# Kernel optimization log

Hardware: AMD Instinct MI355X
Metric: run time of the kernel (lower is better)

Reference implementation:

```python
import jax, jax.numpy as jnp
import numpy as np

FPS, MS = 7, 256
WIDTHS = [(FPS, 12), (12, 12), (12, 12), (12, 12), (12, 12), (12, 6), (6, 1)]


def setup_inputs() -> dict:
    key = jax.random.key(0)
    keys = jax.random.split(key, 1 + 2 * len(WIDTHS))
    B = 32768
    inp = {"inputs": jax.random.normal(keys[0], (B, MS, FPS), dtype=jnp.float32)}
    for li, (fan_in, fan_out) in enumerate(WIDTHS):
        scale = 1.0 / np.sqrt(fan_in)
        inp[f"W{li}"] = jax.random.uniform(keys[1 + 2 * li], (fan_in, fan_out), dtype=jnp.float32, minval=-scale, maxval=scale)
        inp[f"b{li}"] = jnp.zeros((fan_out,), dtype=jnp.float32)
    return inp


def _mlp(x, Ws, bs):
    # layer 0: linear activation
    h = x @ Ws[0] + bs[0]
    # layers 1-4: relu
    for li in range(1, 5):
        h = jax.nn.relu(h @ Ws[li] + bs[li])
    # layer 5: linear (6 units), layer 6: final linear (1 unit)
    h = h @ Ws[5] + bs[5]
    h = h @ Ws[6] + bs[6]
    return h


def reference(inputs, W0, b0, W1, b1, W2, b2, W3, b3, W4, b4, W5, b5, W6, b6):
    B = inputs.shape[0]
    Ws = [W0, W1, W2, W3, W4, W5, W6]
    bs = [b0, b1, b2, b3, b4, b5, b6]
    # Equivalent to looping over ms slices with the shared MLP then concatenating:
    # fold the ms dim into the batch, run once, reshape back to [B, ms].
    x = inputs.reshape(B * MS, FPS)
    out = _mlp(x, Ws, bs)  # [B*MS, 1]
    return out.reshape(B, MS)
```

## Files before the change

### kernel.cpp

```cpp
#include <hip/hip_runtime.h>

#define R 4
#define NTHREADS 256


__global__ __launch_bounds__(NTHREADS, 4) void mlp_kernel(
    const float* __restrict__ in,
    const float* __restrict__ W0, const float* __restrict__ b0,
    const float* __restrict__ W1, const float* __restrict__ b1,
    const float* __restrict__ W2, const float* __restrict__ b2,
    const float* __restrict__ W3, const float* __restrict__ b3,
    const float* __restrict__ W4, const float* __restrict__ b4,
    const float* __restrict__ W5, const float* __restrict__ b5,
    const float* __restrict__ W6, const float* __restrict__ b6,
    float* __restrict__ out, int nrows)
{
    __shared__ __align__(16) float lds[768];
    const int tid = threadIdx.x;

#define STAGE(off, src, count) \
    for (int k = tid; k < (count); k += NTHREADS) lds[(off) + k] = (src)[k];
    STAGE(0,   W0, 84)  STAGE(96,  b0, 12)
    STAGE(112, W1, 144) STAGE(256, b1, 12)
    STAGE(272, W2, 144) STAGE(416, b2, 12)
    STAGE(432, W3, 144) STAGE(576, b3, 12)
    STAGE(592, W4, 144) STAGE(736, b4, 12)
#undef STAGE
    if (tid < 12) {
        float acc = 0.0f;
        for (int c = 0; c < 6; ++c) acc = fmaf(W5[tid * 6 + c], W6[c], acc);
        lds[752 + tid] = acc;
    } else if (tid == 12) {
        float acc = b6[0];
        for (int c = 0; c < 6; ++c) acc = fmaf(b5[c], W6[c], acc);
        lds[764] = acc;
    }
    __syncthreads();

    const long t = (long)blockIdx.x * NTHREADS + tid;
    const long row0 = t * R;
    if (row0 >= nrows) return;
    const bool full = (row0 + R) <= nrows;

    float xs[28];
    if (full) {
        const float4* ip = (const float4*)(in + row0 * 7);
        float4 q;
        q = ip[0]; xs[0]=q.x;  xs[1]=q.y;  xs[2]=q.z;  xs[3]=q.w;
        q = ip[1]; xs[4]=q.x;  xs[5]=q.y;  xs[6]=q.z;  xs[7]=q.w;
        q = ip[2]; xs[8]=q.x;  xs[9]=q.y;  xs[10]=q.z; xs[11]=q.w;
        q = ip[3]; xs[12]=q.x; xs[13]=q.y; xs[14]=q.z; xs[15]=q.w;
        q = ip[4]; xs[16]=q.x; xs[17]=q.y; xs[18]=q.z; xs[19]=q.w;
        q = ip[5]; xs[20]=q.x; xs[21]=q.y; xs[22]=q.z; xs[23]=q.w;
        q = ip[6]; xs[24]=q.x; xs[25]=q.y; xs[26]=q.z; xs[27]=q.w;
    } else {
        #pragma unroll
        for (int r = 0; r < R; ++r)
            #pragma unroll
            for (int i = 0; i < 7; ++i)
                xs[r * 7 + i] = ((row0 + r) < nrows) ? in[(row0 + r) * 7 + i] : 0.0f;
    }

#define LOADW12(dst, baseptr) { \
    const float4* _p = (const float4*)(baseptr); \
    float4 _a = _p[0], _b = _p[1], _c = _p[2]; \
    dst[0]=_a.x; dst[1]=_a.y; dst[2]=_a.z;  dst[3]=_a.w; \
    dst[4]=_b.x; dst[5]=_b.y; dst[6]=_b.z;  dst[7]=_b.w; \
    dst[8]=_c.x; dst[9]=_c.y; dst[10]=_c.z; dst[11]=_c.w; }

    float h[R][12];

    {
        float bb[12]; LOADW12(bb, lds + 96);
        float w[12];  LOADW12(w, lds + 0);
        #pragma unroll
        for (int r = 0; r < R; ++r)
            #pragma unroll
            for (int j = 0; j < 12; ++j)
                h[r][j] = fmaf(xs[r * 7 + 0], w[j], bb[j]);
        #pragma unroll
        for (int i = 1; i < 7; ++i) {
            LOADW12(w, lds + i * 12);
            #pragma unroll
            for (int r = 0; r < R; ++r)
                #pragma unroll
                for (int j = 0; j < 12; ++j)
                    h[r][j] = fmaf(xs[r * 7 + i], w[j], h[r][j]);
        }
    }

    constexpr int WOFF[4] = {112, 272, 432, 592};
    constexpr int BOFF[4] = {256, 416, 576, 736};
    #pragma unroll
    for (int li = 0; li < 4; ++li) {
        float nxt[R][12];
        {
            float bb[12]; LOADW12(bb, lds + BOFF[li]);
            float w[12];  LOADW12(w, lds + WOFF[li]);
            #pragma unroll
            for (int r = 0; r < R; ++r)
                #pragma unroll
                for (int j = 0; j < 12; ++j)
                    nxt[r][j] = fmaf(h[r][0], w[j], bb[j]);
        }
        #pragma unroll
        for (int i = 1; i < 12; ++i) {
            float w[12]; LOADW12(w, lds + WOFF[li] + i * 12);
            #pragma unroll
            for (int r = 0; r < R; ++r)
                #pragma unroll
                for (int j = 0; j < 12; ++j)
                    nxt[r][j] = fmaf(h[r][i], w[j], nxt[r][j]);
        }
        #pragma unroll
        for (int r = 0; r < R; ++r)
            #pragma unroll
            for (int j = 0; j < 12; ++j)
                h[r][j] = fmaxf(nxt[r][j], 0.0f);
    }

    float w56[12]; LOADW12(w56, lds + 752);
    const float b56 = lds[764];
    float o[R];
    #pragma unroll
    for (int r = 0; r < R; ++r) {
        float acc = fmaf(h[r][0], w56[0], b56);
        #pragma unroll
        for (int i = 1; i < 12; ++i) acc = fmaf(h[r][i], w56[i], acc);
        o[r] = acc;
    }

    if (full) {
        *((float4*)(out + row0)) = make_float4(o[0], o[1], o[2], o[3]);
    } else {
        #pragma unroll
        for (int r = 0; r < R; ++r)
            if ((row0 + r) < nrows) out[row0 + r] = o[r];
    }
#undef LOADW12
}

extern "C" void kernel_launch(void* const* d_in, const int* in_sizes, int n_in,
                              void* d_out, int out_size, void* d_ws, size_t ws_size,
                              hipStream_t stream) {
    const float* in = (const float*)d_in[0];
    const float* W0 = (const float*)d_in[1];  const float* b0 = (const float*)d_in[2];
    const float* W1 = (const float*)d_in[3];  const float* b1 = (const float*)d_in[4];
    const float* W2 = (const float*)d_in[5];  const float* b2 = (const float*)d_in[6];
    const float* W3 = (const float*)d_in[7];  const float* b3 = (const float*)d_in[8];
    const float* W4 = (const float*)d_in[9];  const float* b4 = (const float*)d_in[10];
    const float* W5 = (const float*)d_in[11]; const float* b5 = (const float*)d_in[12];
    const float* W6 = (const float*)d_in[13]; const float* b6 = (const float*)d_in[14];
    float* out = (float*)d_out;

    const int nrows = in_sizes[0] / 7;
    const long nthreads_total = ((long)nrows + R - 1) / R;
    const int blocks = (int)((nthreads_total + NTHREADS - 1) / NTHREADS);

    hipLaunchKernelGGL(mlp_kernel, dim3(blocks), dim3(NTHREADS), 0, stream,
                       in, W0, b0, W1, b1, W2, b2, W3, b3, W4, b4, W5, b5, W6, b6,
                       out, nrows);
}
```

Baseline: 128.3 us.

## Read MLP weights via uniform scalar loads instead of LDS staging

```diff
diff --git a/kernel.cpp b/kernel.cpp
--- a/kernel.cpp
+++ b/kernel.cpp
@@ -3,41 +3,38 @@
 #define R 4
 #define NTHREADS 256
 
+__global__ void fuse56_kernel(const float* __restrict__ W5, const float* __restrict__ b5,
+                              const float* __restrict__ W6, const float* __restrict__ b6,
+                              float* __restrict__ ws) {
+    const int t = threadIdx.x;
+    if (t < 12) {
+        float acc = 0.0f;
+        #pragma unroll
+        for (int c = 0; c < 6; ++c) acc = fmaf(W5[t * 6 + c], W6[c], acc);
+        ws[t] = acc;
+    } else if (t == 12) {
+        float acc = b6[0];
+        #pragma unroll
+        for (int c = 0; c < 6; ++c) acc = fmaf(b5[c], W6[c], acc);
+        ws[12] = acc;
+    }
+}
 
 __global__ __launch_bounds__(NTHREADS, 4) void mlp_kernel(
     const float* __restrict__ in,
     const float* __restrict__ W0, const float* __restrict__ b0,
-    const float* __restrict__ W1, const float* __restrict__ b1,
-    const float* __restrict__ W2, const float* __restrict__ b2,
-    const float* __restrict__ W3, const float* __restrict__ b3,
-    const float* __restrict__ W4, const float* __restrict__ b4,
-    const float* __restrict__ W5, const float* __restrict__ b5,
-    const float* __restrict__ W6, const float* __restrict__ b6,
+    const float* __restrict__ W1,
+    const float* __restrict__ W2,
+    const float* __restrict__ W3,
+    const float* __restrict__ W4,
+    const float* __restrict__ b1,
+    const float* __restrict__ b2,
+    const float* __restrict__ b3,
+    const float* __restrict__ b4,
+    const float* __restrict__ w56,
     float* __restrict__ out, int nrows)
 {
-    __shared__ __align__(16) float lds[768];
-    const int tid = threadIdx.x;
-
-#define STAGE(off, src, count) \
-    for (int k = tid; k < (count); k += NTHREADS) lds[(off) + k] = (src)[k];
-    STAGE(0,   W0, 84)  STAGE(96,  b0, 12)
-    STAGE(112, W1, 144) STAGE(256, b1, 12)
-    STAGE(272, W2, 144) STAGE(416, b2, 12)
-    STAGE(432, W3, 144) STAGE(576, b3, 12)
-    STAGE(592, W4, 144) STAGE(736, b4, 12)
-#undef STAGE
-    if (tid < 12) {
-        float acc = 0.0f;
-        for (int c = 0; c < 6; ++c) acc = fmaf(W5[tid * 6 + c], W6[c], acc);
-        lds[752 + tid] = acc;
-    } else if (tid == 12) {
-        float acc = b6[0];
-        for (int c = 0; c < 6; ++c) acc = fmaf(b5[c], W6[c], acc);
-        lds[764] = acc;
-    }
-    __syncthreads();
-
-    const long t = (long)blockIdx.x * NTHREADS + tid;
+    const long t = (long)blockIdx.x * NTHREADS + threadIdx.x;
     const long row0 = t * R;
     if (row0 >= nrows) return;
     const bool full = (row0 + R) <= nrows;
@@ -61,56 +58,53 @@
                 xs[r * 7 + i] = ((row0 + r) < nrows) ? in[(row0 + r) * 7 + i] : 0.0f;
     }
 
-#define LOADW12(dst, baseptr) { \
-    const float4* _p = (const float4*)(baseptr); \
-    float4 _a = _p[0], _b = _p[1], _c = _p[2]; \
-    dst[0]=_a.x; dst[1]=_a.y; dst[2]=_a.z;  dst[3]=_a.w; \
-    dst[4]=_b.x; dst[5]=_b.y; dst[6]=_b.z;  dst[7]=_b.w; \
-    dst[8]=_c.x; dst[9]=_c.y; dst[10]=_c.z; dst[11]=_c.w; }
-
     float h[R][12];
 
     {
-        float bb[12]; LOADW12(bb, lds + 96);
-        float w[12];  LOADW12(w, lds + 0);
         #pragma unroll
-        for (int r = 0; r < R; ++r)
+        for (int j = 0; j < 12; ++j) {
+            const float wv = W0[j];
+            const float bv = b0[j];
             #pragma unroll
-            for (int j = 0; j < 12; ++j)
-                h[r][j] = fmaf(xs[r * 7 + 0], w[j], bb[j]);
+            for (int r = 0; r < R; ++r)
+                h[r][j] = fmaf(xs[r * 7 + 0], wv, bv);
+        }
         #pragma unroll
         for (int i = 1; i < 7; ++i) {
-            LOADW12(w, lds + i * 12);
             #pragma unroll
-            for (int r = 0; r < R; ++r)
+            for (int j = 0; j < 12; ++j) {
+                const float wv = W0[i * 12 + j];
                 #pragma unroll
-                for (int j = 0; j < 12; ++j)
-                    h[r][j] = fmaf(xs[r * 7 + i], w[j], h[r][j]);
+                for (int r = 0; r < R; ++r)
+                    h[r][j] = fmaf(xs[r * 7 + i], wv, h[r][j]);
+            }
         }
     }
 
-    constexpr int WOFF[4] = {112, 272, 432, 592};
-    constexpr int BOFF[4] = {256, 416, 576, 736};
+    const float* __restrict__ Ws[4] = {W1, W2, W3, W4};
+    const float* __restrict__ Bs[4] = {b1, b2, b3, b4};
     #pragma unroll
     for (int li = 0; li < 4; ++li) {
+        const float* __restrict__ Wl = Ws[li];
+        const float* __restrict__ Bl = Bs[li];
         float nxt[R][12];
-        {
-            float bb[12]; LOADW12(bb, lds + BOFF[li]);
-            float w[12];  LOADW12(w, lds + WOFF[li]);
+        #pragma unroll
+        for (int j = 0; j < 12; ++j) {
+            const float wv = Wl[j];
+            const float bv = Bl[j];
             #pragma unroll
             for (int r = 0; r < R; ++r)
-                #pragma unroll
-                for (int j = 0; j < 12; ++j)
-                    nxt[r][j] = fmaf(h[r][0], w[j], bb[j]);
+                nxt[r][j] = fmaf(h[r][0], wv, bv);
         }
         #pragma unroll
         for (int i = 1; i < 12; ++i) {
-            float w[12]; LOADW12(w, lds + WOFF[li] + i * 12);
             #pragma unroll
-            for (int r = 0; r < R; ++r)
+            for (int j = 0; j < 12; ++j) {
+                const float wv = Wl[i * 12 + j];
                 #pragma unroll
-                for (int j = 0; j < 12; ++j)
-                    nxt[r][j] = fmaf(h[r][i], w[j], nxt[r][j]);
+                for (int r = 0; r < R; ++r)
+                    nxt[r][j] = fmaf(h[r][i], wv, nxt[r][j]);
+            }
         }
         #pragma unroll
         for (int r = 0; r < R; ++r)
@@ -119,15 +113,15 @@
                 h[r][j] = fmaxf(nxt[r][j], 0.0f);
     }
 
-    float w56[12]; LOADW12(w56, lds + 752);
-    const float b56 = lds[764];
+    const float b56 = w56[12];
     float o[R];
     #pragma unroll
-    for (int r = 0; r < R; ++r) {
-        float acc = fmaf(h[r][0], w56[0], b56);
+    for (int r = 0; r < R; ++r) o[r] = fmaf(h[r][0], w56[0], b56);
+    #pragma unroll
+    for (int i = 1; i < 12; ++i) {
+        const float wv = w56[i];
         #pragma unroll
-        for (int i = 1; i < 12; ++i) acc = fmaf(h[r][i], w56[i], acc);
-        o[r] = acc;
+        for (int r = 0; r < R; ++r) o[r] = fmaf(h[r][i], wv, o[r]);
     }
 
     if (full) {
@@ -137,7 +131,6 @@
         for (int r = 0; r < R; ++r)
             if ((row0 + r) < nrows) out[row0 + r] = o[r];
     }
-#undef LOADW12
 }
 
 extern "C" void kernel_launch(void* const* d_in, const int* in_sizes, int n_in,
@@ -152,12 +145,15 @@
     const float* W5 = (const float*)d_in[11]; const float* b5 = (const float*)d_in[12];
     const float* W6 = (const float*)d_in[13]; const float* b6 = (const float*)d_in[14];
     float* out = (float*)d_out;
+    float* ws = (float*)d_ws;
+
+    hipLaunchKernelGGL(fuse56_kernel, dim3(1), dim3(64), 0, stream, W5, b5, W6, b6, ws);
 
     const int nrows = in_sizes[0] / 7;
     const long nthreads_total = ((long)nrows + R - 1) / R;
     const int blocks = (int)((nthreads_total + NTHREADS - 1) / NTHREADS);
 
     hipLaunchKernelGGL(mlp_kernel, dim3(blocks), dim3(NTHREADS), 0, stream,
-                       in, W0, b0, W1, b1, W2, b2, W3, b3, W4, b4, W5, b5, W6, b6,
+                       in, W0, b0, W1, W2, W3, W4, b1, b2, b3, b4, ws,
                        out, nrows);
 }
```

Result: slower. 163.8 us (+27.7%).
